# Kernel tuning notes

Measured on AMD Instinct MI355X. Metric: run time of the kernel, lower is better.

Reference implementation:

```python
import jax, jax.numpy as jnp
import numpy as np

EPS = 1e-5
HEADS = 16
HEAD_DIM = 64
SIG_SCALE = HEAD_DIM ** (-0.25)
DEFAULT_BIAS = -3.0

def layernorm(x, scale, offset):
    mu = jnp.mean(x, axis=-1, keepdims=True)
    var = jnp.mean(jnp.square(x - mu), axis=-1, keepdims=True)
    return (x - mu) * jax.lax.rsqrt(var + EPS) * scale + offset

def setup_inputs() -> dict:
    key = jax.random.key(0)
    ks = jax.random.split(key, 16)
    B, Nq, Nk, D, A = 2, 2048, 2048, 1024, 1024
    s = 0.02
    return {
        "query_feats": jax.random.normal(ks[0], (B, Nq, D), jnp.float32),
        "key_feats": jax.random.normal(ks[1], (B, Nk, D), jnp.float32),
        "Wq": jax.random.normal(ks[2], (A, D), jnp.float32) * s,
        "Wk": jax.random.normal(ks[3], (A, D), jnp.float32) * s,
        "Wv": jax.random.normal(ks[4], (A, D), jnp.float32) * s,
        "Wo": jax.random.normal(ks[5], (D, A), jnp.float32) * s,
        "qn_scale": jnp.ones((HEAD_DIM,), jnp.float32),
        "qn_bias": jnp.zeros((HEAD_DIM,), jnp.float32),
        "kn_scale": jnp.ones((HEAD_DIM,), jnp.float32),
        "kn_bias": jnp.zeros((HEAD_DIM,), jnp.float32),
        "ln_q_scale": jnp.ones((D,), jnp.float32),
        "ln_q_bias": jnp.zeros((D,), jnp.float32),
        "ln_out_scale": jnp.ones((D,), jnp.float32),
        "ln_out_bias": jnp.zeros((D,), jnp.float32),
        "gamma": jnp.full((D,), 1e-5, jnp.float32),
    }

def reference(query_feats, key_feats, Wq, Wk, Wv, Wo, qn_scale, qn_bias, kn_scale, kn_bias, ln_q_scale, ln_q_bias, ln_out_scale, ln_out_bias, gamma):
    B, Nq, _ = query_feats.shape
    Nk = key_feats.shape[1]
    residual = query_feats
    xq = layernorm(query_feats, ln_q_scale, ln_q_bias)  # norm_first
    # projections (torch Linear: x @ W.T)
    q = (xq @ Wq.T).reshape(B, Nq, HEADS, HEAD_DIM).transpose(0, 2, 1, 3)
    k = (key_feats @ Wk.T).reshape(B, Nk, HEADS, HEAD_DIM).transpose(0, 2, 1, 3)
    v = (key_feats @ Wv.T).reshape(B, Nk, HEADS, HEAD_DIM).transpose(0, 2, 1, 3)
    # qk-norm over head_dim, then fixed sigmoid scale
    q = layernorm(q, qn_scale, qn_bias) * SIG_SCALE
    k = layernorm(k, kn_scale, kn_bias) * SIG_SCALE
    scores = jnp.einsum('bhqd,bhkd->bhqk', q, k) + DEFAULT_BIAS
    # hardware-optimized sigmoid: 0.5*(1+tanh(0.5*x))
    attn = 0.5 * (1.0 + jnp.tanh(0.5 * scores))
    ctx = jnp.einsum('bhqk,bhkd->bhqd', attn, v)
    ctx = ctx.transpose(0, 2, 1, 3).reshape(B, Nq, HEADS * HEAD_DIM)
    out = ctx @ Wo.T
    out = gamma * out
    out = residual + out
    out = layernorm(out, ln_out_scale, ln_out_bias)  # post_norm
    return out
```

## Files before the change

kernel.cpp:

```cpp
#include <hip/hip_runtime.h>

typedef unsigned short u16;
typedef unsigned int u32;
typedef __bf16 bf16x8 __attribute__((ext_vector_type(8)));
typedef float f32x4 __attribute__((ext_vector_type(4)));
typedef float f32x16 __attribute__((ext_vector_type(16)));
typedef u16 u16x8 __attribute__((ext_vector_type(8)));
typedef u16 u16x4 __attribute__((ext_vector_type(4)));
typedef u32 u32x2 __attribute__((ext_vector_type(2)));
typedef u32 u32x4 __attribute__((ext_vector_type(4)));

#define LN_EPS 1e-5f
#define SIG_SCALE_F 0.35355339059327379f
#define NLOG2E -1.4426950408889634f
#define BIAS_L2E 4.328085122666891f

__device__ __forceinline__ u16 f2bf(float f) {
    u32 u = __builtin_bit_cast(u32, f);
    u32 r = u + 0x7fffu + ((u >> 16) & 1u);
    return (u16)(r >> 16);
}
__device__ __forceinline__ float bf2f(u16 v) {
    return __builtin_bit_cast(float, (u32)v << 16);
}
__device__ __forceinline__ u32 pk_hi(float a, float b) {
    return __builtin_amdgcn_perm(__builtin_bit_cast(u32, b), __builtin_bit_cast(u32, a),
                                 0x07060302u);
}

__device__ __forceinline__ void gload16(const u16* g, u16* lds) {
    __builtin_amdgcn_global_load_lds(
        (const __attribute__((address_space(1))) u32*)g,
        (__attribute__((address_space(3))) u32*)lds, 16, 0, 0);
}

__device__ __forceinline__ void gemm_core(f32x4 acc[4][4],
                                          const u16* __restrict__ A, const u16* __restrict__ B,
                                          int Kiter, int lda, int ldb,
                                          long m0, long n0, u16* As, u16* Bs) {
    const int tid = threadIdx.x;
    const int lane = tid & 63;
    const int wave = tid >> 6;
    const int r15 = lane & 15;
    const int qd = lane >> 4;
    const int wm = (wave >> 1) * 64;
    const int wn = (wave & 1) * 64;

    const int srow = wave * 16 + (lane >> 2);
    const int c0 = (lane & 3) ^ (srow & 3);
    const u16* Ap0 = A + (m0 + srow) * lda + c0 * 8;
    const u16* Ap1 = A + (m0 + srow + 64) * lda + c0 * 8;
    const u16* Bp0 = B + (n0 + srow) * ldb + c0 * 8;
    const u16* Bp1 = B + (n0 + srow + 64) * ldb + c0 * 8;
    u16* As0 = As + wave * 512;
    u16* As1 = As + (wave + 4) * 512;
    u16* Bs0 = Bs + wave * 512;
    u16* Bs1 = Bs + (wave + 4) * 512;

    for (int kt = 0; kt < Kiter; kt += 32) {
        __syncthreads();
        gload16(Ap0 + kt, As0);
        gload16(Ap1 + kt, As1);
        gload16(Bp0 + kt, Bs0);
        gload16(Bp1 + kt, Bs1);
        __syncthreads();
        bf16x8 af[4], bfr[4];
#pragma unroll
        for (int i = 0; i < 4; i++) {
            int row = wm + i * 16 + r15;
            af[i] = *(const bf16x8*)(As + row * 32 + ((qd ^ (row & 3)) * 8));
        }
#pragma unroll
        for (int j = 0; j < 4; j++) {
            int row = wn + j * 16 + r15;
            bfr[j] = *(const bf16x8*)(Bs + row * 32 + ((qd ^ (row & 3)) * 8));
        }
#pragma unroll
        for (int i = 0; i < 4; i++)
#pragma unroll
            for (int j = 0; j < 4; j++)
                acc[i][j] = __builtin_amdgcn_mfma_f32_16x16x32_bf16(af[i], bfr[j], acc[i][j], 0, 0, 0);
    }
}

__global__ __launch_bounds__(256, 3) void gemm_qkv(const u16* __restrict__ xq, const u16* __restrict__ keyb,
                                                   const u16* __restrict__ Wqb, const u16* __restrict__ Wkb,
                                                   const u16* __restrict__ Wvb,
                                                   const float* __restrict__ qns, const float* __restrict__ qnb,
                                                   const float* __restrict__ kns, const float* __restrict__ knb,
                                                   u16* __restrict__ qln, u16* __restrict__ kln,
                                                   u16* __restrict__ vt) {
    __shared__ __attribute__((aligned(16))) u16 As[128 * 32];
    __shared__ __attribute__((aligned(16))) u16 Bs[128 * 32];
    const int z = blockIdx.z;
    const u16* A = (z == 0) ? xq : keyb;
    const u16* B = (z == 0) ? Wqb : ((z == 1) ? Wkb : Wvb);
    const long m0 = (long)blockIdx.x * 128;
    const long n0 = (long)blockIdx.y * 128;

    f32x4 acc[4][4];
#pragma unroll
    for (int i = 0; i < 4; i++)
#pragma unroll
        for (int j = 0; j < 4; j++) acc[i][j] = (f32x4){0.f, 0.f, 0.f, 0.f};

    gemm_core(acc, A, B, 1024, 1024, 1024, m0, n0, As, Bs);

    const int lane = threadIdx.x & 63;
    const int wave = threadIdx.x >> 6;
    const int r15 = lane & 15;
    const int qd = lane >> 4;
    const int wm = (wave >> 1) * 64;
    const int wn = (wave & 1) * 64;

    if (z <= 1) {
        u16* C = (z == 0) ? qln : kln;
        const float* sc_ = (z == 0) ? qns : kns;
        const float* bs_ = (z == 0) ? qnb : knb;
        float scl[4], bia[4];
#pragma unroll
        for (int j = 0; j < 4; j++) {
            scl[j] = sc_[j * 16 + r15] * SIG_SCALE_F;
            bia[j] = bs_[j * 16 + r15] * SIG_SCALE_F;
        }
#pragma unroll
        for (int i = 0; i < 4; i++) {
#pragma unroll
            for (int rr = 0; rr < 4; rr++) {
                float a0 = acc[i][0][rr], a1 = acc[i][1][rr], a2 = acc[i][2][rr], a3 = acc[i][3][rr];
                float s1 = (a0 + a1) + (a2 + a3);
                float s2 = __builtin_fmaf(a3, a3,
                           __builtin_fmaf(a2, a2, __builtin_fmaf(a1, a1, a0 * a0)));
#pragma unroll
                for (int off = 1; off <= 8; off <<= 1) {
                    s1 += __shfl_xor(s1, off, 64);
                    s2 += __shfl_xor(s2, off, 64);
                }
                float mu = s1 * (1.0f / 64.0f);
                float var = __builtin_fmaf(-mu, mu, s2 * (1.0f / 64.0f));
                float rs = rsqrtf(var + LN_EPS);
                long row = m0 + wm + i * 16 + qd * 4 + rr;
#pragma unroll
                for (int j = 0; j < 4; j++) {
                    long col = n0 + wn + j * 16 + r15;
                    float o = __builtin_fmaf((acc[i][j][rr] - mu) * rs, scl[j], bia[j]);
                    C[row * 1024 + col] = f2bf(o);
                }
            }
        }
    } else {
#pragma unroll
        for (int i = 0; i < 4; i++)
#pragma unroll
            for (int rr = 0; rr < 4; rr++) {
                int grow = (int)(m0 + wm + i * 16 + qd * 4 + rr);
                int bb = grow >> 11;
                int kk = grow & 2047;
#pragma unroll
                for (int j = 0; j < 4; j++) {
                    int col = (int)(n0 + wn + j * 16 + r15);
                    int hh = col >> 6;
                    int dd = col & 63;
                    vt[((size_t)(bb * 16 + hh) * 64 + dd) * 2048 + kk] = f2bf(acc[i][j][rr]);
                }
            }
    }
}

__global__ __launch_bounds__(256, 4) void gemm_o(const u16* __restrict__ ctx, const u16* __restrict__ Wob,
                                                 u16* __restrict__ opre) {
    __shared__ __attribute__((aligned(16))) u16 As[128 * 32];
    __shared__ __attribute__((aligned(16))) u16 Bs[128 * 32];
    const int z = blockIdx.z;
    const int koff = z * 256;
    u16* C = opre + (size_t)z * 4194304;
    const long m0 = (long)blockIdx.x * 128;
    const long n0 = (long)blockIdx.y * 128;
    f32x4 acc[4][4];
#pragma unroll
    for (int i = 0; i < 4; i++)
#pragma unroll
        for (int j = 0; j < 4; j++) acc[i][j] = (f32x4){0.f, 0.f, 0.f, 0.f};
    gemm_core(acc, ctx + koff, Wob + koff, 256, 1024, 1024, m0, n0, As, Bs);

    const int lane = threadIdx.x & 63;
    const int wave = threadIdx.x >> 6;
    const int r15 = lane & 15;
    const int qd = lane >> 4;
    const int wm = (wave >> 1) * 64;
    const int wn = (wave & 1) * 64;
#pragma unroll
    for (int i = 0; i < 4; i++)
#pragma unroll
        for (int rr = 0; rr < 4; rr++) {
            long row = m0 + wm + i * 16 + qd * 4 + rr;
#pragma unroll
            for (int j = 0; j < 4; j++)
                C[row * 1024 + n0 + wn + j * 16 + r15] = f2bf(acc[i][j][rr]);
        }
}

__device__ __forceinline__ bf16x8 frag64(const u16* base, int row, int kidx) {
    return *(const bf16x8*)(base + row * 64 + ((kidx ^ (row & 7)) * 8));
}

__global__ __launch_bounds__(512, 4) void attn_sigmoid_v8(const u16* __restrict__ q,
                                                          const u16* __restrict__ k,
                                                          const u16* __restrict__ vt,
                                                          u16* __restrict__ ctx) {
    __shared__ __attribute__((aligned(16))) u16 Sh[8192 + 16384 + 16384];
    u16* Qs = Sh;
    u16* Ks = Sh + 8192;
    u16* Vs = Sh + 8192 + 16384;
    float* Obuf = (float*)(Sh + 8192);

    const int tid = threadIdx.x;
    const int lane = tid & 63;
    const int wave = tid >> 6;
    const int l31 = lane & 31;
    const int h = lane >> 5;
    const int qsub = wave & 3;
    const int kh = wave >> 2;
    const int hd = blockIdx.x;
    const int q0 = blockIdx.y * 128;
    const int b = blockIdx.z;
    const int bh = b * 16 + hd;

    const int lr0 = lane >> 3;
    const int lc0 = lane & 7;
    const int wsub = wave & 3;
    const int kbeg = kh * 1024;

    auto stageKV = [&](int cur, int kc) {
#pragma unroll
        for (int i = 0; i < 2; i++) {
            int s = wsub * 2 + i;
            int row = s * 8 + lr0;
            int c = lc0 ^ (row & 7);
            gload16(k + (size_t)(b * 2048 + kc + row) * 1024 + hd * 64 + c * 8,
                    Ks + (cur * 2 + kh) * 4096 + s * 512);
            gload16(vt + (size_t)(bh * 64 + row) * 2048 + kc + c * 8,
                    Vs + (cur * 2 + kh) * 4096 + s * 512);
        }
    };

    {
#pragma unroll
        for (int i = 0; i < 2; i++) {
            int s = wave * 2 + i;
            int row = s * 8 + lr0;
            int c = lc0 ^ (row & 7);
            gload16(q + (size_t)(b * 2048 + q0 + row) * 1024 + hd * 64 + c * 8, Qs + s * 512);
        }
        stageKV(0, kbeg);
    }
    __syncthreads();
    bf16x8 qB[4];
#pragma unroll
    for (int dblk = 0; dblk < 4; dblk++)
        qB[dblk] = frag64(Qs, qsub * 32 + l31, dblk * 2 + h);

    f32x16 accO[2];
#pragma unroll
    for (int dt = 0; dt < 2; dt++)
#pragma unroll
        for (int r = 0; r < 16; r++) accO[dt][r] = 0.f;

    int cur = 0;
    for (int it = 0; it < 16; ++it) {
        const int kc = kbeg + it * 64;
        if (it < 15) stageKV(cur ^ 1, kc + 64);
        const u16* Ksh = Ks + (cur * 2 + kh) * 4096;
        const u16* Vsh = Vs + (cur * 2 + kh) * 4096;

        f32x16 accS[2];
        __builtin_amdgcn_s_setprio(1);
#pragma unroll
        for (int mt = 0; mt < 2; mt++) {
#pragma unroll
            for (int r = 0; r < 16; r++) accS[mt][r] = 0.f;
#pragma unroll
            for (int dblk = 0; dblk < 4; dblk++) {
                bf16x8 aK = frag64(Ksh, mt * 32 + l31, dblk * 2 + h);
                accS[mt] = __builtin_amdgcn_mfma_f32_32x32x16_bf16(aK, qB[dblk], accS[mt], 0, 0, 0);
            }
        }
        __builtin_amdgcn_s_setprio(0);

        u32 pg[2][4][2];
#pragma unroll
        for (int mt = 0; mt < 2; mt++)
#pragma unroll
            for (int g = 0; g < 4; g++) {
                float p[4];
#pragma unroll
                for (int e = 0; e < 4; e++) {
                    float t = __builtin_fmaf(accS[mt][g * 4 + e], NLOG2E, BIAS_L2E);
                    float u = __builtin_amdgcn_exp2f(t);
                    p[e] = __builtin_amdgcn_rcpf(1.0f + u);
                }
                pg[mt][g][0] = pk_hi(p[0], p[1]);
                pg[mt][g][1] = pk_hi(p[2], p[3]);
            }

        __builtin_amdgcn_s_setprio(1);
#pragma unroll
        for (int mt = 0; mt < 2; mt++)
#pragma unroll
            for (int kblk = 0; kblk < 2; kblk++) {
                int glo = kblk * 2, ghi = kblk * 2 + 1;
                u32x2 r0 = __builtin_amdgcn_permlane32_swap(pg[mt][glo][0], pg[mt][ghi][0], false, false);
                u32x2 r1 = __builtin_amdgcn_permlane32_swap(pg[mt][glo][1], pg[mt][ghi][1], false, false);
                u32x4 fr;
                fr[0] = r0[0];
                fr[1] = r1[0];
                fr[2] = r0[1];
                fr[3] = r1[1];
                bf16x8 aP = __builtin_bit_cast(bf16x8, fr);
#pragma unroll
                for (int dt = 0; dt < 2; dt++) {
                    bf16x8 bV = frag64(Vsh, dt * 32 + l31, mt * 4 + kblk * 2 + h);
                    accO[dt] = __builtin_amdgcn_mfma_f32_32x32x16_bf16(aP, bV, accO[dt], 0, 0, 0);
                }
            }
        __builtin_amdgcn_s_setprio(0);

        __syncthreads();
        cur ^= 1;
    }

    if (kh == 1) {
#pragma unroll
        for (int dt = 0; dt < 2; dt++)
#pragma unroll
            for (int r = 0; r < 16; r++) {
                int ql = qsub * 32 + (r & 3) + 8 * (r >> 2) + 4 * h;
                Obuf[ql * 64 + dt * 32 + l31] = accO[dt][r];
            }
    }
    __syncthreads();
    if (kh == 0) {
#pragma unroll
        for (int dt = 0; dt < 2; dt++)
#pragma unroll
            for (int r = 0; r < 16; r++) {
                int ql = qsub * 32 + (r & 3) + 8 * (r >> 2) + 4 * h;
                float s = accO[dt][r] + Obuf[ql * 64 + dt * 32 + l31];
                ctx[(size_t)(b * 2048 + q0 + ql) * 1024 + hd * 64 + dt * 32 + l31] = f2bf(s);
            }
    }
}

__global__ __launch_bounds__(256) void prep(const float* __restrict__ w0, const float* __restrict__ w1,
                                            const float* __restrict__ w2, const float* __restrict__ w3,
                                            const float* __restrict__ kf, const float* __restrict__ qf,
                                            const float* __restrict__ lnq_s, const float* __restrict__ lnq_b,
                                            u16* __restrict__ wdst, u16* __restrict__ kdst,
                                            u16* __restrict__ xq) {
    const int bx = blockIdx.x;
    const int tid = threadIdx.x;
    if (bx < 6144) {
        size_t e = ((size_t)bx * 256 + tid) * 4;
        const float* src;
        u16* dst;
        if (e < 4194304) {
            src = ((e >> 20) == 0 ? w0 : (e >> 20) == 1 ? w1 : (e >> 20) == 2 ? w2 : w3) + (e & 1048575);
            dst = wdst + e;
        } else {
            size_t off = e - 4194304;
            src = kf + off;
            dst = kdst + off;
        }
        float4 xv = *(const float4*)src;
        u16x4 o;
        o[0] = f2bf(xv.x);
        o[1] = f2bf(xv.y);
        o[2] = f2bf(xv.z);
        o[3] = f2bf(xv.w);
        *(u16x4*)dst = o;
    } else {
        __shared__ float s1buf[4], s2buf[4];
        const int row = bx - 6144;
        const size_t base = (size_t)row * 1024 + tid * 4;
        const float4 xv = *(const float4*)(qf + base);
        float s1 = xv.x + xv.y + xv.z + xv.w;
        float s2 = xv.x * xv.x + xv.y * xv.y + xv.z * xv.z + xv.w * xv.w;
        int lane = tid & 63, wave = tid >> 6;
#pragma unroll
        for (int off = 32; off > 0; off >>= 1) {
            s1 += __shfl_down(s1, off, 64);
            s2 += __shfl_down(s2, off, 64);
        }
        if (lane == 0) { s1buf[wave] = s1; s2buf[wave] = s2; }
        __syncthreads();
        s1 = s1buf[0] + s1buf[1] + s1buf[2] + s1buf[3];
        s2 = s2buf[0] + s2buf[1] + s2buf[2] + s2buf[3];
        float mu = s1 * (1.0f / 1024.0f);
        float var = s2 * (1.0f / 1024.0f) - mu * mu;
        float rs = rsqrtf(var + LN_EPS);
        const float4 scv = *(const float4*)(lnq_s + tid * 4);
        const float4 bsv = *(const float4*)(lnq_b + tid * 4);
        u16x4 o;
        o[0] = f2bf((xv.x - mu) * rs * scv.x + bsv.x);
        o[1] = f2bf((xv.y - mu) * rs * scv.y + bsv.y);
        o[2] = f2bf((xv.z - mu) * rs * scv.z + bsv.z);
        o[3] = f2bf((xv.w - mu) * rs * scv.w + bsv.w);
        *(u16x4*)(xq + base) = o;
    }
}

__global__ __launch_bounds__(256) void final_ln(const float* __restrict__ resid,
                                                const u16* __restrict__ opre,
                                                const float* __restrict__ gamma,
                                                const float* __restrict__ sc,
                                                const float* __restrict__ bs,
                                                float* __restrict__ out) {
    __shared__ float s1buf[4], s2buf[4];
    const int row = blockIdx.x;
    const int tid = threadIdx.x;
    const size_t base = (size_t)row * 1024 + tid * 4;
    float4 rv = *(const float4*)(resid + base);
    u16x4 p0 = *(const u16x4*)(opre + base);
    u16x4 p1 = *(const u16x4*)(opre + 4194304 + base);
    u16x4 p2 = *(const u16x4*)(opre + 8388608 + base);
    u16x4 p3 = *(const u16x4*)(opre + 12582912 + base);
    float4 gv = *(const float4*)(gamma + tid * 4);
    float4 xv;
    xv.x = rv.x + gv.x * ((bf2f(p0[0]) + bf2f(p1[0])) + (bf2f(p2[0]) + bf2f(p3[0])));
    xv.y = rv.y + gv.y * ((bf2f(p0[1]) + bf2f(p1[1])) + (bf2f(p2[1]) + bf2f(p3[1])));
    xv.z = rv.z + gv.z * ((bf2f(p0[2]) + bf2f(p1[2])) + (bf2f(p2[2]) + bf2f(p3[2])));
    xv.w = rv.w + gv.w * ((bf2f(p0[3]) + bf2f(p1[3])) + (bf2f(p2[3]) + bf2f(p3[3])));
    float s1 = xv.x + xv.y + xv.z + xv.w;
    float s2 = xv.x * xv.x + xv.y * xv.y + xv.z * xv.z + xv.w * xv.w;
    int lane = tid & 63, wave = tid >> 6;
#pragma unroll
    for (int off = 32; off > 0; off >>= 1) {
        s1 += __shfl_down(s1, off, 64);
        s2 += __shfl_down(s2, off, 64);
    }
    if (lane == 0) { s1buf[wave] = s1; s2buf[wave] = s2; }
    __syncthreads();
    s1 = s1buf[0] + s1buf[1] + s1buf[2] + s1buf[3];
    s2 = s2buf[0] + s2buf[1] + s2buf[2] + s2buf[3];
    float mu = s1 * (1.0f / 1024.0f);
    float var = s2 * (1.0f / 1024.0f) - mu * mu;
    float rs = rsqrtf(var + LN_EPS);
    const float4 scv = *(const float4*)(sc + tid * 4);
    const float4 bsv = *(const float4*)(bs + tid * 4);
    float4 o;
    o.x = (xv.x - mu) * rs * scv.x + bsv.x;
    o.y = (xv.y - mu) * rs * scv.y + bsv.y;
    o.z = (xv.z - mu) * rs * scv.z + bsv.z;
    o.w = (xv.w - mu) * rs * scv.w + bsv.w;
    *(float4*)(out + base) = o;
}

extern "C" void kernel_launch(void* const* d_in, const int* in_sizes, int n_in,
                              void* d_out, int out_size, void* d_ws, size_t ws_size,
                              hipStream_t stream) {
    const float* qf    = (const float*)d_in[0];
    const float* kf    = (const float*)d_in[1];
    const float* Wq    = (const float*)d_in[2];
    const float* Wk    = (const float*)d_in[3];
    const float* Wv    = (const float*)d_in[4];
    const float* Wo    = (const float*)d_in[5];
    const float* qn_s  = (const float*)d_in[6];
    const float* qn_b  = (const float*)d_in[7];
    const float* kn_s  = (const float*)d_in[8];
    const float* kn_b  = (const float*)d_in[9];
    const float* lnq_s = (const float*)d_in[10];
    const float* lnq_b = (const float*)d_in[11];
    const float* lno_s = (const float*)d_in[12];
    const float* lno_b = (const float*)d_in[13];
    const float* gamma = (const float*)d_in[14];
    float* out = (float*)d_out;

    char* ws = (char*)d_ws;
    const size_t MB = 1024 * 1024;
    u16* Wqb   = (u16*)(ws + 0 * MB);
    u16* Wkb   = (u16*)(ws + 2 * MB);
    u16* Wvb   = (u16*)(ws + 4 * MB);
    u16* Wob   = (u16*)(ws + 6 * MB);
    u16* xq    = (u16*)(ws + 8 * MB);
    u16* ctx   = (u16*)(ws + 8 * MB);
    u16* keyb  = (u16*)(ws + 16 * MB);
    u16* qln   = (u16*)(ws + 24 * MB);
    u16* kln   = (u16*)(ws + 32 * MB);
    u16* vt    = (u16*)(ws + 48 * MB);
    u16* opre  = (u16*)(ws + 24 * MB);

    prep<<<dim3(10240), 256, 0, stream>>>(Wq, Wk, Wv, Wo, kf, qf, lnq_s, lnq_b, Wqb, keyb, xq);

    gemm_qkv<<<dim3(32, 8, 3), 256, 0, stream>>>(xq, keyb, Wqb, Wkb, Wvb,
                                                 qn_s, qn_b, kn_s, kn_b, qln, kln, vt);

    attn_sigmoid_v8<<<dim3(16, 16, 2), 512, 0, stream>>>(qln, kln, vt, ctx);

    gemm_o<<<dim3(32, 8, 4), 256, 0, stream>>>(ctx, Wob, opre);
    final_ln<<<dim3(4096), 256, 0, stream>>>(qf, opre, gamma, lno_s, lno_b, out);
}
```

Before: 227.3 us.

## Software-pipeline attention loop: overlap S MFMA with sigmoid and PV of previous tile

Restructures the attention inner loop into a two-stage software pipeline: the QK^T MFMA for tile i+1 is issued alongside the PV MFMA and sigmoid of tile i, with a triple-buffered V staging area that reuses the Q shared-memory region. It also folds the -log2(e) factor into the Q layernorm scale and preloads the bias into the S accumulator, removing an FMA per score. This is meant to hide transcendental latency behind matrix-core work, at the cost of extra registers (two P buffers) and more intricate buffer indexing.

After: 345.4 us. 1.52x slower.

```diff
diff --git a/kernel.cpp b/kernel.cpp
--- a/kernel.cpp
+++ b/kernel.cpp
@@ -117,11 +117,12 @@
         u16* C = (z == 0) ? qln : kln;
         const float* sc_ = (z == 0) ? qns : kns;
         const float* bs_ = (z == 0) ? qnb : knb;
+        const float post = (z == 0) ? SIG_SCALE_F * NLOG2E : SIG_SCALE_F;
         float scl[4], bia[4];
 #pragma unroll
         for (int j = 0; j < 4; j++) {
-            scl[j] = sc_[j * 16 + r15] * SIG_SCALE_F;
-            bia[j] = bs_[j * 16 + r15] * SIG_SCALE_F;
+            scl[j] = sc_[j * 16 + r15] * post;
+            bia[j] = bs_[j * 16 + r15] * post;
         }
 #pragma unroll
         for (int i = 0; i < 4; i++) {
@@ -204,7 +205,7 @@
     return *(const bf16x8*)(base + row * 64 + ((kidx ^ (row & 7)) * 8));
 }
 
-__global__ __launch_bounds__(512, 4) void attn_sigmoid_v8(const u16* __restrict__ q,
+__global__ __launch_bounds__(512, 4) void attn_sigmoid_v9(const u16* __restrict__ q,
                                                           const u16* __restrict__ k,
                                                           const u16* __restrict__ vt,
                                                           u16* __restrict__ ctx) {
@@ -231,16 +232,19 @@
     const int wsub = wave & 3;
     const int kbeg = kh * 1024;
 
-    auto stageKV = [&](int cur, int kc) {
+    auto kptr = [&](int slot) { return Ks + (slot * 2 + kh) * 4096; };
+    auto vptr = [&](int slot) { return (slot == 2 ? Sh : Vs + slot * 8192) + kh * 4096; };
+
+    auto stageKV = [&](int kslot, int vslot, int kc) {
+        u16* kd = kptr(kslot);
+        u16* vd = vptr(vslot);
 #pragma unroll
         for (int i = 0; i < 2; i++) {
             int s = wsub * 2 + i;
             int row = s * 8 + lr0;
             int c = lc0 ^ (row & 7);
-            gload16(k + (size_t)(b * 2048 + kc + row) * 1024 + hd * 64 + c * 8,
-                    Ks + (cur * 2 + kh) * 4096 + s * 512);
-            gload16(vt + (size_t)(bh * 64 + row) * 2048 + kc + c * 8,
-                    Vs + (cur * 2 + kh) * 4096 + s * 512);
+            gload16(k + (size_t)(b * 2048 + kc + row) * 1024 + hd * 64 + c * 8, kd + s * 512);
+            gload16(vt + (size_t)(bh * 64 + row) * 2048 + kc + c * 8, vd + s * 512);
         }
     };
 
@@ -252,7 +256,7 @@
             int c = lc0 ^ (row & 7);
             gload16(q + (size_t)(b * 2048 + q0 + row) * 1024 + hd * 64 + c * 8, Qs + s * 512);
         }
-        stageKV(0, kbeg);
+        stageKV(0, 0, kbeg);
     }
     __syncthreads();
     bf16x8 qB[4];
@@ -266,19 +270,16 @@
 #pragma unroll
         for (int r = 0; r < 16; r++) accO[dt][r] = 0.f;
 
-    int cur = 0;
-    for (int it = 0; it < 16; ++it) {
-        const int kc = kbeg + it * 64;
-        if (it < 15) stageKV(cur ^ 1, kc + 64);
-        const u16* Ksh = Ks + (cur * 2 + kh) * 4096;
-        const u16* Vsh = Vs + (cur * 2 + kh) * 4096;
-
-        f32x16 accS[2];
+    f32x16 accS[2];
+    u32 pgA[2][4][2], pgB[2][4][2];
+
+    auto do_S = [&](int kslot) {
+        const u16* Ksh = kptr(kslot);
         __builtin_amdgcn_s_setprio(1);
 #pragma unroll
         for (int mt = 0; mt < 2; mt++) {
 #pragma unroll
-            for (int r = 0; r < 16; r++) accS[mt][r] = 0.f;
+            for (int r = 0; r < 16; r++) accS[mt][r] = BIAS_L2E;
 #pragma unroll
             for (int dblk = 0; dblk < 4; dblk++) {
                 bf16x8 aK = frag64(Ksh, mt * 32 + l31, dblk * 2 + h);
@@ -286,8 +287,8 @@
             }
         }
         __builtin_amdgcn_s_setprio(0);
-
-        u32 pg[2][4][2];
+    };
+    auto do_sig = [&](u32 (&pg)[2][4][2]) {
 #pragma unroll
         for (int mt = 0; mt < 2; mt++)
 #pragma unroll
@@ -295,14 +296,15 @@
                 float p[4];
 #pragma unroll
                 for (int e = 0; e < 4; e++) {
-                    float t = __builtin_fmaf(accS[mt][g * 4 + e], NLOG2E, BIAS_L2E);
-                    float u = __builtin_amdgcn_exp2f(t);
+                    float u = __builtin_amdgcn_exp2f(accS[mt][g * 4 + e]);
                     p[e] = __builtin_amdgcn_rcpf(1.0f + u);
                 }
                 pg[mt][g][0] = pk_hi(p[0], p[1]);
                 pg[mt][g][1] = pk_hi(p[2], p[3]);
             }
-
+    };
+    auto do_PV = [&](const u32 (&pg)[2][4][2], int vslot) {
+        const u16* Vsh = vptr(vslot);
         __builtin_amdgcn_s_setprio(1);
 #pragma unroll
         for (int mt = 0; mt < 2; mt++)
@@ -324,10 +326,37 @@
                 }
             }
         __builtin_amdgcn_s_setprio(0);
-
-        __syncthreads();
-        cur ^= 1;
-    }
+    };
+
+    stageKV(1, 1, kbeg + 64);
+    do_S(0);
+    do_sig(pgB);
+    __syncthreads();
+
+#pragma unroll 1
+    for (int p = 0; p < 7; ++p) {
+        const int it = 1 + 2 * p;
+        {
+            stageKV(0, (it + 1) % 3, kbeg + (it + 1) * 64);
+            do_S(1);
+            do_PV(pgB, (it - 1) % 3);
+            do_sig(pgA);
+            __syncthreads();
+        }
+        {
+            stageKV(1, (it + 3) % 3, kbeg + (it + 2) * 64);
+            do_S(0);
+            do_PV(pgA, it % 3);
+            do_sig(pgB);
+            __syncthreads();
+        }
+    }
+
+    do_S(1);
+    do_PV(pgB, 2);
+    do_sig(pgA);
+    do_PV(pgA, 0);
+    __syncthreads();
 
     if (kh == 1) {
 #pragma unroll
@@ -494,7 +523,7 @@
     gemm_qkv<<<dim3(32, 8, 3), 256, 0, stream>>>(xq, keyb, Wqb, Wkb, Wvb,
                                                  qn_s, qn_b, kn_s, kn_b, qln, kln, vt);
 
-    attn_sigmoid_v8<<<dim3(16, 16, 2), 512, 0, stream>>>(qln, kln, vt, ctx);
+    attn_sigmoid_v9<<<dim3(16, 16, 2), 512, 0, stream>>>(qln, kln, vt, ctx);
 
     gemm_o<<<dim3(32, 8, 4), 256, 0, stream>>>(ctx, Wob, opre);
     final_ln<<<dim3(4096), 256, 0, stream>>>(qf, opre, gamma, lno_s, lno_b, out);
```
